# Performance work log

Hardware: AMD Instinct MI355X
Metric: run time of the kernel (lower is better)

## Reference

```python
import jax, jax.numpy as jnp
import numpy as np

B, HH, WW, E = 8, 128, 128, 192
NH = 8
D1 = (3 * E) // NH * NH  # 576
HD = D1 // NH            # 72
RPE = 512
LAYERS = 3
EPS = 1e-8


def srms(x):
    # SimpleRMSNorm: x / (||x||_2 / sqrt(d) + eps), no learned params
    d = x.shape[-1]
    norm = jnp.linalg.norm(x, axis=-1, keepdims=True)
    return x / (norm * (d ** -0.5) + EPS)


def rpe_net(idx, pos_w, pos_b, lw, lb, out_w, out_b):
    # idx: (L, 1) float positions -> (NH, L, HD) Toeplitz coefficients
    h = idx @ pos_w.T + pos_b  # (L, RPE)
    for i in range(LAYERS):   # residual=False
        h = jax.nn.relu(srms(h)) @ lw[i].T + lb[i]
    h = jax.nn.relu(srms(h)) @ out_w.T + out_b  # (L, NH*HD)
    return h.reshape(idx.shape[0], NH, HD).transpose(1, 0, 2)


def tno(v, axis, pos_w, pos_b, lw, lb, out_w, out_b):
    # v: (b, h, H, W, d); Toeplitz mixing along `axis` (-3 or -2), non-causal,
    # par_type=1, no decay, act_type='none', normalize=False.
    n = v.shape[axis]
    z = jnp.zeros((1,), jnp.float32)
    p = jnp.arange(1, n, dtype=jnp.float32)
    # coefficient layout for length-2n circular conv: a0, a1..a(n-1), a0, a-(n-1)..a-1
    idx = jnp.concatenate([z, p, z, -p[::-1]]).reshape(-1, 1)  # (2n, 1)
    a = rpe_net(idx, pos_w, pos_b, lw, lb, out_w, out_b)       # (NH, 2n, HD)
    ak = a[:, None, :, :] if axis == -2 else a[:, :, None, :]
    y = jnp.fft.rfft(v, 2 * n, axis=axis)
    af = jnp.fft.rfft(ak, 2 * n, axis=axis)
    out = jnp.fft.irfft(af * y, 2 * n, axis=axis)
    return out[..., :n, :] if axis == -2 else out[..., :n, :, :]


def setup_inputs() -> dict:
    key = jax.random.key(0)
    ks = jax.random.split(key, 19)
    s = 0.02
    rn = lambda k, shape, sc=s: jax.random.normal(k, shape, dtype=jnp.float32) * sc
    inp = {
        'x': jax.random.normal(ks[0], (B, HH, WW, E), dtype=jnp.float32),
        'u_w': rn(ks[1], (D1, E)), 'u_b': rn(ks[2], (D1,)),
        'v_w': rn(ks[3], (D1, E)), 'v_b': rn(ks[4], (D1,)),
        'o_w': rn(ks[5], (E, D1)), 'o_b': rn(ks[6], (E,)),
    }
    for i, name in enumerate(['rpe1', 'rpe2']):
        off = 7 + i * 6
        inp[name + '_pos_w'] = rn(ks[off], (RPE, 1), 0.5)
        inp[name + '_pos_b'] = rn(ks[off + 1], (RPE,), 0.5)
        inp[name + '_lw'] = rn(ks[off + 2], (LAYERS, RPE, RPE))
        inp[name + '_lb'] = rn(ks[off + 3], (LAYERS, RPE))
        inp[name + '_out_w'] = rn(ks[off + 4], (NH * HD, RPE))
        inp[name + '_out_b'] = rn(ks[off + 5], (NH * HD,))
    inp['H'] = HH
    inp['W'] = WW
    return inp


def reference(x, u_w, u_b, v_w, v_b, o_w, o_b,
              rpe1_pos_w, rpe1_pos_b, rpe1_lw, rpe1_lb, rpe1_out_w, rpe1_out_b,
              rpe2_pos_w, rpe2_pos_b, rpe2_lw, rpe2_lb, rpe2_out_w, rpe2_out_b,
              H, W):
    shortcut = x
    xn = srms(x)                              # pre_norm (SimpleRMSNorm)
    u = jax.nn.silu(xn @ u_w.T + u_b)         # (B,H,W,D1)
    v = jax.nn.silu(xn @ v_w.T + v_b)
    b = v.shape[0]
    v = v.reshape(b, H, W, NH, HD).transpose(0, 3, 1, 2, 4)  # b h H W d
    out = (tno(v, -3, rpe2_pos_w, rpe2_pos_b, rpe2_lw, rpe2_lb, rpe2_out_w, rpe2_out_b)
           + tno(v, -2, rpe1_pos_w, rpe1_pos_b, rpe1_lw, rpe1_lb, rpe1_out_w, rpe1_out_b))
    out = out.transpose(0, 2, 3, 1, 4).reshape(b, H, W, NH * HD)  # b H W (h d)
    out = u * out
    return out @ o_w.T + o_b + shortcut
```

## Files before the change

### kernel.cpp

```cpp
#include <hip/hip_runtime.h>
#include <hip/hip_bf16.h>

typedef __hip_bfloat16 bf16;
typedef __attribute__((ext_vector_type(4))) float f32x4;
typedef __attribute__((ext_vector_type(8))) __bf16 bf16x8;
typedef __attribute__((ext_vector_type(4))) __bf16 bf16x4;

constexpr int NB  = 8;
constexpr int NHH = 128;
constexpr int NWW = 128;
constexpr int NE  = 192;
constexpr int ND  = 576;
constexpr int NR  = 512;
constexpr int NL  = 256;
constexpr int NP  = NB * NHH * NWW;
constexpr int NPC = NHH * NWW;

__device__ __forceinline__ void gload16(const void* g, void* l) {
    __builtin_amdgcn_global_load_lds(
        (const __attribute__((address_space(1))) unsigned int*)g,
        (__attribute__((address_space(3))) unsigned int*)l, 16, 0, 0);
}

__global__ __launch_bounds__(256) void k_pre1(
    const float* __restrict__ pw1, const float* __restrict__ pb1,
    const float* __restrict__ pw2, const float* __restrict__ pb2,
    const float* __restrict__ lw1, const float* __restrict__ ow1,
    const float* __restrict__ lw2, const float* __restrict__ ow2,
    float* __restrict__ h, float* __restrict__ wt)
{
    __shared__ float tile[32][33];
    int b = blockIdx.x;
    if (b < 512) {
        int net = b >> 8, l = b & 255;
        const float* pw = net ? pw2 : pw1;
        const float* pb = net ? pb2 : pb1;
        float idxv;
        if (l == 0 || l == 128) idxv = 0.f;
        else if (l < 128)       idxv = (float)l;
        else                    idxv = (float)(l - 256);
        float* hr = h + ((size_t)net * NL + l) * NR;
        for (int r = threadIdx.x; r < NR; r += 256)
            hr[r] = idxv * pw[r] + pb[r];
    } else {
        int idx = b - 512;
        int m = idx / 288;
        int rem = idx - m * 288;
        int jb = rem >> 4, rb = rem & 15;
        int net = m >> 2, sub = m & 3;
        int J = (sub == 3) ? 576 : 512;
        const float* src = (sub == 3) ? (net ? ow2 : ow1)
                                      : (net ? lw2 : lw1) + (size_t)sub * 262144;
        float* dst = wt + (size_t)net * 1081344 + ((sub == 3) ? 786432 : sub * 262144);
        int r0 = rb * 32, j0 = jb * 32;
        if (j0 >= J) return;
        int tx = threadIdx.x & 31, ty = threadIdx.x >> 5;
        #pragma unroll
        for (int d = 0; d < 4; ++d) {
            int j = j0 + ty + d * 8;
            tile[ty + d * 8][tx] = (j < J) ? src[(size_t)j * 512 + r0 + tx] : 0.f;
        }
        __syncthreads();
        #pragma unroll
        for (int d = 0; d < 4; ++d) {
            int r = r0 + ty + d * 8;
            int j = j0 + tx;
            if (j < J) dst[(size_t)r * J + j] = tile[tx][ty + d * 8];
        }
    }
}

__global__ __launch_bounds__(256) void k_rpe_layer(
    const float* __restrict__ hin,
    const float* __restrict__ Wt1, const float* __restrict__ b1,
    const float* __restrict__ Wt2, const float* __restrict__ b2,
    float* __restrict__ out1, float* __restrict__ out2, int outdim)
{
    __shared__ float g[2][NR];
    __shared__ float red[256];
    int net = blockIdx.x >> 7;
    int l0  = (blockIdx.x & 127) * 2;
    const float* hr = hin + ((size_t)net * NL + l0) * NR;
    int tid = threadIdx.x;
    int row = tid >> 7, ix = tid & 127;
    const float* hh = hr + (size_t)row * NR;
    float a0 = hh[ix], a1 = hh[ix + 128], a2 = hh[ix + 256], a3 = hh[ix + 384];
    red[tid] = a0 * a0 + a1 * a1 + a2 * a2 + a3 * a3;
    __syncthreads();
    for (int off = 64; off; off >>= 1) {
        if (ix < off) red[tid] += red[tid + off];
        __syncthreads();
    }
    float sc = 1.f / (sqrtf(red[row << 7]) * 0.044194173824159216f + 1e-8f);
    g[row][ix]       = fmaxf(a0 * sc, 0.f);
    g[row][ix + 128] = fmaxf(a1 * sc, 0.f);
    g[row][ix + 256] = fmaxf(a2 * sc, 0.f);
    g[row][ix + 384] = fmaxf(a3 * sc, 0.f);
    __syncthreads();
    const float* Wt = net ? Wt2 : Wt1;
    const float* bb = net ? b2 : b1;
    float* o0 = (net ? out2 : out1) + (size_t)l0 * outdim;
    int half = outdim >> 1;
    for (int jj = tid; jj < half; jj += 256) {
        float ax0 = 0.f, ay0 = 0.f, ax1 = 0.f, ay1 = 0.f;
        const float* wp = Wt + 2 * jj;
        #pragma unroll 8
        for (int r = 0; r < NR; ++r) {
            float2 w = *(const float2*)(wp + (size_t)r * outdim);
            float g0 = g[0][r], g1 = g[1][r];
            ax0 = fmaf(g0, w.x, ax0); ay0 = fmaf(g0, w.y, ay0);
            ax1 = fmaf(g1, w.x, ax1); ay1 = fmaf(g1, w.y, ay1);
        }
        float bx = bb[2 * jj], by = bb[2 * jj + 1];
        o0[2 * jj]              = ax0 + bx;  o0[2 * jj + 1]          = ay0 + by;
        o0[outdim + 2 * jj]     = ax1 + bx;  o0[outdim + 2 * jj + 1] = ay1 + by;
    }
}

__global__ __launch_bounds__(256) void k_pre2(
    const float* __restrict__ x, bf16* __restrict__ xbn,
    const float* __restrict__ A1, const float* __restrict__ A2, bf16* __restrict__ T,
    const float* __restrict__ uw, const float* __restrict__ vw,
    const float* __restrict__ ow, bf16* __restrict__ wb, bf16* __restrict__ owb)
{
    __shared__ __align__(16) char sm[17408];
    int b = blockIdx.x;
    int tid = threadIdx.x;
    if (b < 32768) {
        __bf16 (*wbuf)[208] = (__bf16(*)[208])sm;
        int w = tid >> 6, lane = tid & 63;
        int p = b * 4 + w;
        const float* xp = x + (size_t)p * NE;
        float v0 = xp[lane], v1 = xp[lane + 64], v2 = xp[lane + 128];
        float ss = v0 * v0 + v1 * v1 + v2 * v2;
        for (int off = 32; off; off >>= 1) ss += __shfl_xor(ss, off, 64);
        float sc = __builtin_amdgcn_rcpf(sqrtf(ss) * 0.07216878364870323f + 1e-8f);
        wbuf[w][lane]       = (__bf16)(v0 * sc);
        wbuf[w][lane + 64]  = (__bf16)(v1 * sc);
        wbuf[w][lane + 128] = (__bf16)(v2 * sc);
        __syncthreads();
        if (lane < 24) {
            bf16x8 o = *(bf16x8*)&wbuf[w][lane * 8];
            int t = (lane & 24) | ((lane & 7) ^ (p & 7));
            *(bf16x8*)((__bf16*)xbn + (size_t)p * NE + t * 8) = o;
        }
    } else if (b < 32768 + 288) {
        float (*Als)[17] = (float(*)[17])sm;
        int i = b - 32768;
        int cb = i % 36, rq = (i / 36) & 3, net = i / 144;
        const float* A = net ? A2 : A1;
        #pragma unroll
        for (int it = 0; it < 16; ++it) {
            int el = it * 256 + tid;
            int k = el >> 4, cl = el & 15;
            Als[k][cl] = A[(size_t)k * ND + cb * 16 + cl];
        }
        __syncthreads();
        int cl = tid >> 4, sg = tid & 15;
        __bf16* Tb = (__bf16*)T + (((size_t)net * ND + cb * 16 + cl) * 128) * 128;
        for (int rr = 0; rr < 32; ++rr) {
            int r = rq * 32 + rr;
            bf16x8 o;
            #pragma unroll
            for (int j = 0; j < 8; ++j)
                o[j] = (__bf16)Als[(r - sg * 8 - j) & 255][cl];
            *(bf16x8*)(Tb + (size_t)r * 128 + sg * 8) = o;
        }
    } else {
        int gid = (b - 33056) * 256 + tid;
        if (gid < 27648) {
            int row = gid / 24, bb = gid - row * 24;
            const float* src = ((row < ND) ? uw + (size_t)row * NE
                                           : vw + (size_t)(row - ND) * NE) + bb * 8;
            float4 f0 = ((const float4*)src)[0], f1 = ((const float4*)src)[1];
            bf16x8 o;
            o[0] = (__bf16)f0.x; o[1] = (__bf16)f0.y; o[2] = (__bf16)f0.z; o[3] = (__bf16)f0.w;
            o[4] = (__bf16)f1.x; o[5] = (__bf16)f1.y; o[6] = (__bf16)f1.z; o[7] = (__bf16)f1.w;
            int t = (bb & 24) | ((bb & 7) ^ (row & 7));
            *(bf16x8*)((__bf16*)wb + (size_t)row * NE + t * 8) = o;
        } else if (gid < 27648 + 13824) {
            int g = gid - 27648;
            const float* src = ow + (size_t)g * 8;
            float4 f0 = ((const float4*)src)[0], f1 = ((const float4*)src)[1];
            bf16x8 o;
            o[0] = (__bf16)f0.x; o[1] = (__bf16)f0.y; o[2] = (__bf16)f0.z; o[3] = (__bf16)f0.w;
            o[4] = (__bf16)f1.x; o[5] = (__bf16)f1.y; o[6] = (__bf16)f1.z; o[7] = (__bf16)f1.w;
            *(bf16x8*)((__bf16*)owb + (size_t)g * 8) = o;
        }
    }
}

__global__ __launch_bounds__(256, 4) void k_uv(
    const bf16* __restrict__ xbn, const bf16* __restrict__ wb,
    const float* __restrict__ ub, const float* __restrict__ vb,
    bf16* __restrict__ u_t, bf16* __restrict__ v_t)
{
    __shared__ __align__(16) char smem[33792];
    __bf16 (*sA)[64] = (__bf16(*)[64])smem;
    __bf16 (*sB)[64] = (__bf16(*)[64])(smem + 16384);
    __bf16* ldst = (__bf16*)smem;
    int tid = threadIdx.x;
    int wv = tid >> 6, lane = tid & 63;
    int b = blockIdx.x;
    int chunk = b & 7;
    int s = b >> 3;
    int by = s / 9;
    int ntile = s - by * 9;
    int nbase = ntile * 128;
    int wr = wv >> 1, wc = wv & 1;
    int lrow = lane >> 3, lcol = lane & 7;
    size_t gbase = (size_t)chunk * NPC + by * 128;
    f32x4 acc[4][4] = {};
    for (int kk = 0; kk < 3; ++kk) {
        #pragma unroll
        for (int i = 0; i < 4; ++i) {
            int row = wv * 32 + i * 8;
            gload16((const char*)(xbn + (gbase + row + lrow) * NE + kk * 64) + lcol * 16,
                    &sA[row][0]);
            gload16((const char*)(wb + (size_t)(nbase + row + lrow) * NE + kk * 64) + lcol * 16,
                    &sB[row][0]);
        }
        asm volatile("s_waitcnt vmcnt(0)" ::: "memory");
        __syncthreads();
        int q = lane >> 4, fr = lane & 15;
        #pragma unroll
        for (int k2 = 0; k2 < 2; ++k2) {
            bf16x8 af[4], bw[4];
            #pragma unroll
            for (int m = 0; m < 4; ++m) {
                int frm = wr * 64 + m * 16 + fr;
                af[m] = *(const bf16x8*)&sA[frm][(((k2 << 2) | q) ^ (frm & 7)) * 8];
            }
            #pragma unroll
            for (int n = 0; n < 4; ++n) {
                int fn = wc * 64 + n * 16 + fr;
                bw[n] = *(const bf16x8*)&sB[fn][(((k2 << 2) | q) ^ (fn & 7)) * 8];
            }
            #pragma unroll
            for (int m = 0; m < 4; ++m)
                #pragma unroll
                for (int n = 0; n < 4; ++n)
                    acc[m][n] = __builtin_amdgcn_mfma_f32_16x16x32_bf16(af[m], bw[n], acc[m][n], 0, 0, 0);
        }
        __syncthreads();
    }
    int fr = lane & 15, fq = lane >> 4;
    #pragma unroll
    for (int m = 0; m < 4; ++m) {
        #pragma unroll
        for (int n = 0; n < 4; ++n) {
            int row = wc * 64 + n * 16 + fr;
            int jn_g = nbase + row;
            float bias = (jn_g < ND) ? ub[jn_g] : vb[jn_g - ND];
            bf16x4 val;
            #pragma unroll
            for (int j = 0; j < 4; ++j) {
                float z = acc[m][n][j] + bias;
                float sgl = z * __builtin_amdgcn_rcpf(1.f + __expf(-z));
                val[j] = (__bf16)sgl;
            }
            *(bf16x4*)&ldst[row * 132 + wr * 64 + m * 16 + fq * 4] = val;
        }
    }
    __syncthreads();
    size_t pgl = gbase + (tid & 15) * 8;
    #pragma unroll
    for (int pass = 0; pass < 8; ++pass) {
        int row = (tid >> 4) + pass * 16;
        int jn_g = nbase + row;
        int colb = (tid & 15) * 8;
        bf16x4 a = *(bf16x4*)&ldst[row * 132 + colb];
        bf16x4 bb = *(bf16x4*)&ldst[row * 132 + colb + 4];
        bf16x8 o;
        #pragma unroll
        for (int i = 0; i < 4; ++i) { o[i] = a[i]; o[i + 4] = bb[i]; }
        __bf16* dst = (jn_g < ND) ? (__bf16*)u_t + (size_t)jn_g * NP + pgl
                                  : (__bf16*)v_t + (size_t)(jn_g - ND) * NP + pgl;
        *(bf16x8*)dst = o;
    }
}

__global__ __launch_bounds__(256) void k_conv(
    bf16* __restrict__ v_t, const bf16* __restrict__ T, const bf16* __restrict__ u_t)
{
    __shared__ __bf16 Vp[128][132];
    int tid = threadIdx.x;
    int b = blockIdx.x;
    int c = (b & 7) * 72 + ((b >> 3) >> 3);
    int chunk = (b >> 3) & 7;
    size_t pbase = (size_t)c * NP + (size_t)chunk * NPC;
    const __bf16* vsrc = (const __bf16*)v_t + pbase;
    #pragma unroll
    for (int it = 0; it < 8; ++it) {
        int y = (tid >> 4) + 16 * it;
        int x0 = (tid & 15) * 8;
        bf16x8 rd = __builtin_nontemporal_load((const bf16x8*)(vsrc + (size_t)y * 128 + x0));
        bf16x4 lo, hi;
        #pragma unroll
        for (int i = 0; i < 4; ++i) { lo[i] = rd[i]; hi[i] = rd[i + 4]; }
        *(bf16x4*)&Vp[y][x0]     = lo;
        *(bf16x4*)&Vp[y][x0 + 4] = hi;
    }
    __syncthreads();
    int wv = tid >> 6, lane = tid & 63;
    int wr = wv >> 1, wc = wv & 1;
    int fr = lane & 15, q = lane >> 4;
    const __bf16* T1 = (const __bf16*)T + (size_t)c * 16384;
    const __bf16* T2 = (const __bf16*)T + (size_t)(ND + c) * 16384;
    f32x4 acc[4][4] = {};
    #pragma unroll
    for (int k = 0; k < 4; ++k) {
        bf16x8 af[4], bw[4];
        #pragma unroll
        for (int m = 0; m < 4; ++m) {
            int row = wr * 64 + m * 16 + fr;
            bf16x4 a = *(const bf16x4*)&Vp[row][k * 32 + q * 8];
            bf16x4 bb = *(const bf16x4*)&Vp[row][k * 32 + q * 8 + 4];
            #pragma unroll
            for (int i = 0; i < 4; ++i) { af[m][i] = a[i]; af[m][i + 4] = bb[i]; }
        }
        #pragma unroll
        for (int n = 0; n < 4; ++n)
            bw[n] = *(const bf16x8*)(T1 + (size_t)(wc * 64 + n * 16 + fr) * 128 + k * 32 + q * 8);
        #pragma unroll
        for (int m = 0; m < 4; ++m)
            #pragma unroll
            for (int n = 0; n < 4; ++n)
                acc[m][n] = __builtin_amdgcn_mfma_f32_16x16x32_bf16(af[m], bw[n], acc[m][n], 0, 0, 0);
    }
    #pragma unroll
    for (int k = 0; k < 4; ++k) {
        bf16x8 a2[4], b2[4];
        #pragma unroll
        for (int m = 0; m < 4; ++m)
            a2[m] = *(const bf16x8*)(T2 + (size_t)(wr * 64 + m * 16 + fr) * 128 + k * 32 + q * 8);
        #pragma unroll
        for (int n = 0; n < 4; ++n) {
            int xc = wc * 64 + n * 16 + fr;
            #pragma unroll
            for (int j = 0; j < 8; ++j)
                b2[n][j] = Vp[k * 32 + q * 8 + j][xc];
        }
        #pragma unroll
        for (int m = 0; m < 4; ++m)
            #pragma unroll
            for (int n = 0; n < 4; ++n)
                acc[m][n] = __builtin_amdgcn_mfma_f32_16x16x32_bf16(a2[m], b2[n], acc[m][n], 0, 0, 0);
    }
    __syncthreads();
    #pragma unroll
    for (int m = 0; m < 4; ++m) {
        #pragma unroll
        for (int n = 0; n < 4; ++n) {
            int xc = wc * 64 + n * 16 + fr;
            #pragma unroll
            for (int j = 0; j < 4; ++j) {
                int y = wr * 64 + m * 16 + q * 4 + j;
                Vp[y][xc] = (__bf16)acc[m][n][j];
            }
        }
    }
    __syncthreads();
    const __bf16* usrc = (const __bf16*)u_t + pbase;
    __bf16* vdst = (__bf16*)v_t + pbase;
    #pragma unroll
    for (int it = 0; it < 8; ++it) {
        int y = (tid >> 4) + 16 * it;
        int x0 = (tid & 15) * 8;
        bf16x8 uu = __builtin_nontemporal_load((const bf16x8*)(usrc + (size_t)y * 128 + x0));
        bf16x4 lo = *(const bf16x4*)&Vp[y][x0];
        bf16x4 hi = *(const bf16x4*)&Vp[y][x0 + 4];
        bf16x8 o;
        #pragma unroll
        for (int i = 0; i < 4; ++i) {
            o[i]     = (__bf16)((float)uu[i]     * (float)lo[i]);
            o[i + 4] = (__bf16)((float)uu[i + 4] * (float)hi[i]);
        }
        __builtin_nontemporal_store(o, (bf16x8*)(vdst + (size_t)y * 128 + x0));
    }
}

__global__ __launch_bounds__(256) void k_out(
    const bf16* __restrict__ g_t, const bf16* __restrict__ owb,
    const float* __restrict__ ob, const float* __restrict__ x, float* __restrict__ out)
{
    __shared__ __bf16 gs[64][132];
    int tid = threadIdx.x;
    int b = blockIdx.x;
    int xcd = b & 7, s = b >> 3;
    int eh = s & 1;
    int pt = xcd * 128 + (s >> 1);
    int wv = tid >> 6, lane = tid & 63;
    int wr = wv >> 1, wc = wv & 1;
    int fr = lane & 15, q = lane >> 4;
    int ebase = eh * 96 + wc * 48;
    f32x4 acc[4][3] = {};
    for (int kk = 0; kk < 9; ++kk) {
        #pragma unroll
        for (int i = 0; i < 4; ++i) {
            int cl = (tid >> 4) + 16 * i;
            int pg = (tid & 15) * 8;
            bf16x8 rd = *(const bf16x8*)((const __bf16*)g_t + (size_t)(kk * 64 + cl) * NP
                                         + (size_t)pt * 128 + pg);
            bf16x4 lo, hi;
            #pragma unroll
            for (int ii = 0; ii < 4; ++ii) { lo[ii] = rd[ii]; hi[ii] = rd[ii + 4]; }
            *(bf16x4*)&gs[cl][pg]     = lo;
            *(bf16x4*)&gs[cl][pg + 4] = hi;
        }
        __syncthreads();
        #pragma unroll
        for (int ks = 0; ks < 2; ++ks) {
            bf16x8 af[4], bw[3];
            #pragma unroll
            for (int m = 0; m < 4; ++m) {
                int prow = wr * 64 + m * 16 + fr;
                #pragma unroll
                for (int j = 0; j < 8; ++j)
                    af[m][j] = gs[ks * 32 + q * 8 + j][prow];
            }
            #pragma unroll
            for (int n = 0; n < 3; ++n) {
                int e = ebase + n * 16 + fr;
                bw[n] = *(const bf16x8*)((const __bf16*)owb + (size_t)e * ND + kk * 64 + ks * 32 + q * 8);
            }
            #pragma unroll
            for (int m = 0; m < 4; ++m)
                #pragma unroll
                for (int n = 0; n < 3; ++n)
                    acc[m][n] = __builtin_amdgcn_mfma_f32_16x16x32_bf16(af[m], bw[n], acc[m][n], 0, 0, 0);
        }
        __syncthreads();
    }
    #pragma unroll
    for (int m = 0; m < 4; ++m) {
        #pragma unroll
        for (int n = 0; n < 3; ++n) {
            int e = ebase + n * 16 + fr;
            float bias = ob[e];
            #pragma unroll
            for (int j = 0; j < 4; ++j) {
                size_t p = (size_t)pt * 128 + wr * 64 + m * 16 + q * 4 + j;
                float xv = __builtin_nontemporal_load(x + p * NE + e);
                __builtin_nontemporal_store(acc[m][n][j] + bias + xv, out + p * NE + e);
            }
        }
    }
}

extern "C" void kernel_launch(void* const* d_in, const int* in_sizes, int n_in,
                              void* d_out, int out_size, void* d_ws, size_t ws_size,
                              hipStream_t stream)
{
    const float* x    = (const float*)d_in[0];
    const float* u_w  = (const float*)d_in[1];
    const float* u_b  = (const float*)d_in[2];
    const float* v_w  = (const float*)d_in[3];
    const float* v_b  = (const float*)d_in[4];
    const float* o_w  = (const float*)d_in[5];
    const float* o_b  = (const float*)d_in[6];
    const float* r1_pw = (const float*)d_in[7];
    const float* r1_pb = (const float*)d_in[8];
    const float* r1_lw = (const float*)d_in[9];
    const float* r1_lb = (const float*)d_in[10];
    const float* r1_ow = (const float*)d_in[11];
    const float* r1_ob = (const float*)d_in[12];
    const float* r2_pw = (const float*)d_in[13];
    const float* r2_pb = (const float*)d_in[14];
    const float* r2_lw = (const float*)d_in[15];
    const float* r2_lb = (const float*)d_in[16];
    const float* r2_ow = (const float*)d_in[17];
    const float* r2_ob = (const float*)d_in[18];
    float* out = (float*)d_out;

    float* A1  = (float*)d_ws;
    float* A2  = A1 + (size_t)NL * ND;
    bf16* wb   = (bf16*)(A2 + (size_t)NL * ND);
    bf16* owb  = wb + (size_t)2 * ND * NE;
    bf16* u_t  = owb + (size_t)NE * ND;
    bf16* v_t  = u_t + (size_t)ND * NP;
    bf16* xbn  = v_t + (size_t)ND * NP;
    float* h0 = (float*)(xbn + (size_t)NP * NE);
    float* h1 = h0 + (size_t)2 * NL * NR;
    float* wt = h1 + (size_t)2 * NL * NR;
    bf16* T   = (bf16*)h0;

    k_pre1<<<dim3(2816), dim3(256), 0, stream>>>(
        r1_pw, r1_pb, r2_pw, r2_pb, r1_lw, r1_ow, r2_lw, r2_ow, h0, wt);
    {
        const float* src[3] = { h0, h1, h0 };
        float* dst[3]       = { h1, h0, h1 };
        for (int i = 0; i < 3; ++i) {
            k_rpe_layer<<<dim3(256), dim3(256), 0, stream>>>(
                src[i], wt + (size_t)i * 262144, r1_lb + (size_t)i * NR,
                        wt + 1081344 + (size_t)i * 262144, r2_lb + (size_t)i * NR,
                dst[i], dst[i] + (size_t)NL * NR, NR);
        }
        k_rpe_layer<<<dim3(256), dim3(256), 0, stream>>>(
            h1, wt + 786432, r1_ob, wt + 1081344 + 786432, r2_ob, A1, A2, ND);
    }
    k_pre2<<<dim3(33272), dim3(256), 0, stream>>>(
        x, xbn, A1, A2, T, u_w, v_w, o_w, wb, owb);

    k_uv<<<dim3(9216), dim3(256), 0, stream>>>(xbn, wb, u_b, v_b, u_t, v_t);
    k_conv<<<dim3(4608), dim3(256), 0, stream>>>(v_t, T, u_t);
    k_out<<<dim3(2048), dim3(256), 0, stream>>>(v_t, owb, o_b, x, out);
}
```

Baseline: 532.0 us.

## Split RPE layer matvec across output quarters and reduction lanes

The RPE MLP layer kernel now launches four times as many blocks. Each block handles a quarter of the output columns, and four lanes split the 512-long reduction into 128-element chunks that are combined with xor shuffles. The shared activation buffer is padded with a per-chunk offset so the four lanes do not hit the same LDS bank. This targets the low occupancy of the old 256-block launch, at the cost of recomputing the row norm in each split block and adding shuffle reductions.

```diff
diff --git a/kernel.cpp b/kernel.cpp
--- a/kernel.cpp
+++ b/kernel.cpp
@@ -76,10 +76,13 @@
     const float* __restrict__ Wt2, const float* __restrict__ b2,
     float* __restrict__ out1, float* __restrict__ out2, int outdim)
 {
-    __shared__ float g[2][NR];
+    __shared__ float g[2][NR + 4];
     __shared__ float red[256];
-    int net = blockIdx.x >> 7;
-    int l0  = (blockIdx.x & 127) * 2;
+    int bk = blockIdx.x;
+    int net = bk >> 9;
+    int bb  = bk & 511;
+    int l0    = (bb >> 2) * 2;
+    int split = bb & 3;
     const float* hr = hin + ((size_t)net * NL + l0) * NR;
     int tid = threadIdx.x;
     int row = tid >> 7, ix = tid & 127;
@@ -93,27 +96,40 @@
     }
     float sc = 1.f / (sqrtf(red[row << 7]) * 0.044194173824159216f + 1e-8f);
     g[row][ix]       = fmaxf(a0 * sc, 0.f);
-    g[row][ix + 128] = fmaxf(a1 * sc, 0.f);
-    g[row][ix + 256] = fmaxf(a2 * sc, 0.f);
-    g[row][ix + 384] = fmaxf(a3 * sc, 0.f);
+    g[row][ix + 129] = fmaxf(a1 * sc, 0.f);
+    g[row][ix + 258] = fmaxf(a2 * sc, 0.f);
+    g[row][ix + 387] = fmaxf(a3 * sc, 0.f);
     __syncthreads();
     const float* Wt = net ? Wt2 : Wt1;
-    const float* bb = net ? b2 : b1;
+    const float* bv = net ? b2 : b1;
     float* o0 = (net ? out2 : out1) + (size_t)l0 * outdim;
     int half = outdim >> 1;
-    for (int jj = tid; jj < half; jj += 256) {
+    int quarter = (half + 3) >> 2;
+    int jbase = split * quarter;
+    int rpart = tid & 3;
+    int gofs = rpart * 129;
+    const float* wbase = Wt + (size_t)(rpart * 128) * outdim;
+    for (int jl = tid >> 2; jl < quarter; jl += 64) {
+        int jj = jbase + jl;
+        if (jj >= half) break;
         float ax0 = 0.f, ay0 = 0.f, ax1 = 0.f, ay1 = 0.f;
-        const float* wp = Wt + 2 * jj;
+        const float* wp = wbase + 2 * jj;
         #pragma unroll 8
-        for (int r = 0; r < NR; ++r) {
+        for (int r = 0; r < 128; ++r) {
             float2 w = *(const float2*)(wp + (size_t)r * outdim);
-            float g0 = g[0][r], g1 = g[1][r];
+            float g0 = g[0][gofs + r], g1 = g[1][gofs + r];
             ax0 = fmaf(g0, w.x, ax0); ay0 = fmaf(g0, w.y, ay0);
             ax1 = fmaf(g1, w.x, ax1); ay1 = fmaf(g1, w.y, ay1);
         }
-        float bx = bb[2 * jj], by = bb[2 * jj + 1];
-        o0[2 * jj]              = ax0 + bx;  o0[2 * jj + 1]          = ay0 + by;
-        o0[outdim + 2 * jj]     = ax1 + bx;  o0[outdim + 2 * jj + 1] = ay1 + by;
+        ax0 += __shfl_xor(ax0, 1, 64); ax0 += __shfl_xor(ax0, 2, 64);
+        ay0 += __shfl_xor(ay0, 1, 64); ay0 += __shfl_xor(ay0, 2, 64);
+        ax1 += __shfl_xor(ax1, 1, 64); ax1 += __shfl_xor(ax1, 2, 64);
+        ay1 += __shfl_xor(ay1, 1, 64); ay1 += __shfl_xor(ay1, 2, 64);
+        if (rpart == 0) {
+            float bx = bv[2 * jj], by = bv[2 * jj + 1];
+            o0[2 * jj]              = ax0 + bx;  o0[2 * jj + 1]          = ay0 + by;
+            o0[outdim + 2 * jj]     = ax1 + bx;  o0[outdim + 2 * jj + 1] = ay1 + by;
+        }
     }
 }
 
@@ -491,12 +507,12 @@
         const float* src[3] = { h0, h1, h0 };
         float* dst[3]       = { h1, h0, h1 };
         for (int i = 0; i < 3; ++i) {
-            k_rpe_layer<<<dim3(256), dim3(256), 0, stream>>>(
+            k_rpe_layer<<<dim3(1024), dim3(256), 0, stream>>>(
                 src[i], wt + (size_t)i * 262144, r1_lb + (size_t)i * NR,
                         wt + 1081344 + (size_t)i * 262144, r2_lb + (size_t)i * NR,
                 dst[i], dst[i] + (size_t)NL * NR, NR);
         }
-        k_rpe_layer<<<dim3(256), dim3(256), 0, stream>>>(
+        k_rpe_layer<<<dim3(1024), dim3(256), 0, stream>>>(
             h1, wt + 786432, r1_ob, wt + 1081344 + 786432, r2_ob, A1, A2, ND);
     }
     k_pre2<<<dim3(33272), dim3(256), 0, stream>>>(
```

Result: slower. 645.7 us (+21.4%).
